# Optimization experiments

Measured on AMD Instinct MI355X. Metric: run time of the kernel, lower is better.

Reference implementation:

```python
import jax, jax.numpy as jnp
import numpy as np

SEQ_LEN = 8192
EMBED_DIM = 768
OUTPUT_DIM = 64


def setup_inputs() -> dict:
    key = jax.random.key(0)
    k_in, k_q, k_k, k_v = jax.random.split(key, 4)
    inputs = jax.random.normal(k_in, (SEQ_LEN, EMBED_DIM), dtype=jnp.float32)
    W_Q = jax.random.normal(k_q, (EMBED_DIM, OUTPUT_DIM), dtype=jnp.float32)
    W_K = jax.random.normal(k_k, (EMBED_DIM, OUTPUT_DIM), dtype=jnp.float32)
    W_V = jax.random.normal(k_v, (EMBED_DIM, OUTPUT_DIM), dtype=jnp.float32)
    return {"inputs": inputs, "W_Q": W_Q, "W_K": W_K, "W_V": W_V}


def reference(inputs, W_Q, W_K, W_V):
    # inputs: [N, E]; weights: [E, D]
    queries = inputs @ W_Q              # [N, D]
    keys = inputs @ W_K                 # [N, D]
    values = inputs @ W_V               # [N, D]
    scale = values.shape[-1] ** 0.5     # sqrt(output_dim), as in the original
    scores = queries @ keys.T           # [N, N] -- full score matrix, as original
    weights = jax.nn.softmax(scores / scale, axis=-1)
    context = weights @ values          # [N, D]
    return context
```

## Files before the change

### kernel.cpp

```cpp
#include <hip/hip_runtime.h>
#include <hip/hip_fp16.h>

#define N_SEQ 8192
#define E_DIM 768
#define D_OUT 64
#define PADK 68
#define SCALE_LOG2 0.18033688011112042f

typedef __attribute__((ext_vector_type(8)))  short s16x8;
typedef __attribute__((ext_vector_type(4)))  float f32x4;
typedef __attribute__((ext_vector_type(16))) float f32x16;

static __device__ __forceinline__ unsigned short f2bf(float f) {
    union { float f; unsigned int u; } v; v.f = f;
    unsigned int r = v.u + 0x7FFFu + ((v.u >> 16) & 1u);
    return (unsigned short)(r >> 16);
}
static __device__ __forceinline__ float bf2f(unsigned short h) {
    union { float f; unsigned int u; } v; v.u = ((unsigned int)h) << 16; return v.f;
}
static __device__ __forceinline__ unsigned int packbf(float a, float b) {
    union { float f; unsigned int u; } x, y; x.f = a; y.f = b;
    return (y.u & 0xFFFF0000u) | (x.u >> 16);
}
static __device__ __forceinline__ s16x8 gfrag(const unsigned short* p) {
    union { uint4 u; s16x8 s; } r; r.u = *(const uint4*)p; return r.s;
}
static __device__ __forceinline__ s16x8 ldsfrag(const unsigned short* p) {
    union { uint2 u[2]; s16x8 s; } r;
    r.u[0] = *(const uint2*)(p);
    r.u[1] = *(const uint2*)(p + 4);
    return r.s;
}
static __device__ __forceinline__ void st32(unsigned short* d, uint4 a, uint4 b) {
    uint2* p = (uint2*)d;
    p[0] = make_uint2(a.x, a.y); p[1] = make_uint2(a.z, a.w);
    p[2] = make_uint2(b.x, b.y); p[3] = make_uint2(b.z, b.w);
}

__global__ __launch_bounds__(256) void prep_w(const float* __restrict__ WQ,
                                              const float* __restrict__ WK,
                                              const float* __restrict__ WV,
                                              unsigned short* __restrict__ Wthi,
                                              unsigned short* __restrict__ Wtlo) {
    int idx = blockIdx.x * 256 + threadIdx.x;
    if (idx >= 192 * E_DIM) return;
    int n = idx / E_DIM;
    int k = idx - n * E_DIM;
    float v;
    if (n < 64)       v = WQ[k * 64 + n];
    else if (n < 128) v = WK[k * 64 + (n - 64)];
    else              v = WV[k * 64 + (n - 128)];
    unsigned short hb = f2bf(v);
    Wthi[idx] = hb;
    Wtlo[idx] = f2bf(v - bf2f(hb));
}

__global__ __launch_bounds__(256, 2) void proj_qkv(const float* __restrict__ X,
                                                   const unsigned short* __restrict__ Wthi,
                                                   const unsigned short* __restrict__ Wtlo,
                                                   unsigned short* __restrict__ Qhi,
                                                   unsigned short* __restrict__ Qlo,
                                                   unsigned short* __restrict__ Khi,
                                                   unsigned short* __restrict__ Klo,
                                                   unsigned short* __restrict__ Vt) {
    int tid  = threadIdx.x;
    int wv   = tid >> 6;
    int lane = tid & 63;
    int id   = blockIdx.x * 4 + wv;
    int mt   = id >> 2;
    int c    = id & 3;
    int m0 = mt * 16, n0 = c * 16;
    int lr = lane & 15, lk = lane >> 4;

    f32x4 aQ, aK, aV;
    #pragma unroll
    for (int i = 0; i < 4; ++i) { aQ[i] = 0.f; aK[i] = 0.f; aV[i] = 0.f; }

    const float*          xp  = X    + (size_t)(m0 + lr) * E_DIM + lk * 8;
    const unsigned short* wqh = Wthi + (size_t)(n0 + lr) * E_DIM + lk * 8;
    const unsigned short* wql = Wtlo + (size_t)(n0 + lr) * E_DIM + lk * 8;
    const unsigned short* wkh = Wthi + (size_t)(64 + n0 + lr) * E_DIM + lk * 8;
    const unsigned short* wkl = Wtlo + (size_t)(64 + n0 + lr) * E_DIM + lk * 8;
    const unsigned short* wvh = Wthi + (size_t)(128 + n0 + lr) * E_DIM + lk * 8;

    #pragma unroll 2
    for (int ks = 0; ks < E_DIM / 32; ++ks) {
        int kb = ks * 32;
        float4 x0 = *(const float4*)(xp + kb);
        float4 x1 = *(const float4*)(xp + kb + 4);
        s16x8 bqh = gfrag(wqh + kb);
        s16x8 bql = gfrag(wql + kb);
        s16x8 bkh = gfrag(wkh + kb);
        s16x8 bkl = gfrag(wkl + kb);
        s16x8 bvh = gfrag(wvh + kb);
        float xs[8] = { x0.x, x0.y, x0.z, x0.w, x1.x, x1.y, x1.z, x1.w };
        union { unsigned short u[8]; s16x8 s; } ah, al;
        #pragma unroll
        for (int i = 0; i < 8; ++i) {
            unsigned short hb = f2bf(xs[i]);
            ah.u[i] = hb;
            al.u[i] = f2bf(xs[i] - bf2f(hb));
        }
        aQ = __builtin_amdgcn_mfma_f32_16x16x32_bf16(ah.s, bqh, aQ, 0, 0, 0);
        aK = __builtin_amdgcn_mfma_f32_16x16x32_bf16(ah.s, bkh, aK, 0, 0, 0);
        aV = __builtin_amdgcn_mfma_f32_16x16x32_bf16(ah.s, bvh, aV, 0, 0, 0);
        aQ = __builtin_amdgcn_mfma_f32_16x16x32_bf16(ah.s, bql, aQ, 0, 0, 0);
        aK = __builtin_amdgcn_mfma_f32_16x16x32_bf16(ah.s, bkl, aK, 0, 0, 0);
        aQ = __builtin_amdgcn_mfma_f32_16x16x32_bf16(al.s, bqh, aQ, 0, 0, 0);
        aK = __builtin_amdgcn_mfma_f32_16x16x32_bf16(al.s, bkh, aK, 0, 0, 0);
    }

    #pragma unroll
    for (int r = 0; r < 4; ++r) {
        int grow = m0 + lk * 4 + r, gcol = n0 + lr;
        float q = aQ[r] * SCALE_LOG2;
        unsigned short hb = f2bf(q);
        Qhi[(size_t)grow * 64 + gcol] = hb;
        Qlo[(size_t)grow * 64 + gcol] = f2bf(q - bf2f(hb));
        float v = aK[r];
        hb = f2bf(v);
        Khi[(size_t)grow * 64 + gcol] = hb;
        Klo[(size_t)grow * 64 + gcol] = f2bf(v - bf2f(hb));
    }
    ushort4 pk;
    pk.x = f2bf(aV[0]); pk.y = f2bf(aV[1]);
    pk.z = f2bf(aV[2]); pk.w = f2bf(aV[3]);
    *(ushort4*)(Vt + (size_t)(n0 + lr) * N_SEQ + m0 + lk * 4) = pk;
}

__global__ __launch_bounds__(256, 3) void attn(const unsigned short* __restrict__ Qhi,
                                               const unsigned short* __restrict__ Qlo,
                                               const unsigned short* __restrict__ Khi,
                                               const unsigned short* __restrict__ Klo,
                                               const unsigned short* __restrict__ Vt,
                                               unsigned short* __restrict__ Opart,
                                               float* __restrict__ mpart,
                                               float* __restrict__ lpart,
                                               int chunk) {
    __shared__ unsigned short sK[128 * PADK];
    __shared__ unsigned short sV [64 * PADK];

    int tid = threadIdx.x, wv = tid >> 6, lane = tid & 63;
    int lrow = lane & 31, lh = lane >> 5;
    int c = blockIdx.x, qb = blockIdx.y;
    int q0 = qb * 128 + wv * 32;

    s16x8 qh[4], ql[4];
    #pragma unroll
    for (int ks = 0; ks < 4; ++ks) {
        int kb = ks * 16 + lh * 8;
        qh[ks] = gfrag(Qhi + (size_t)(q0 + lrow) * 64 + kb);
        ql[ks] = gfrag(Qlo + (size_t)(q0 + lrow) * 64 + kb);
    }

    f32x16 O0, O1;
    #pragma unroll
    for (int i = 0; i < 16; ++i) { O0[i] = 0.f; O1[i] = 0.f; }
    float mrow = -1e30f, lrun = 0.f;

    int steps = chunk >> 6;
    int srow = tid >> 2, sseg = tid & 3;

    uint4 rA0, rA1, rB0, rB1, rC0, rC1;
    {
        int j1 = c * chunk;
        const uint4* ps = (const uint4*)(Khi + ((size_t)(j1 + srow) * 64 + sseg * 16));
        rA0 = ps[0]; rA1 = ps[1];
        ps = (const uint4*)(Klo + ((size_t)(j1 + srow) * 64 + sseg * 16));
        rB0 = ps[0]; rB1 = ps[1];
        ps = (const uint4*)(Vt + ((size_t)srow * N_SEQ + j1 + sseg * 16));
        rC0 = ps[0]; rC1 = ps[1];
    }

    for (int it = 0; it < steps; ++it) {
        __syncthreads();
        st32(sK + srow * PADK + sseg * 16, rA0, rA1);
        st32(sK + (64 + srow) * PADK + sseg * 16, rB0, rB1);
        st32(sV + srow * PADK + sseg * 16, rC0, rC1);
        __syncthreads();

        if (it + 1 < steps) {
            int j1 = c * chunk + (it + 1) * 64;
            const uint4* ps = (const uint4*)(Khi + ((size_t)(j1 + srow) * 64 + sseg * 16));
            rA0 = ps[0]; rA1 = ps[1];
            ps = (const uint4*)(Klo + ((size_t)(j1 + srow) * 64 + sseg * 16));
            rB0 = ps[0]; rB1 = ps[1];
            ps = (const uint4*)(Vt + ((size_t)srow * N_SEQ + j1 + sseg * 16));
            rC0 = ps[0]; rC1 = ps[1];
        }

        f32x16 s0, s1;
        #pragma unroll
        for (int i = 0; i < 16; ++i) { s0[i] = 0.f; s1[i] = 0.f; }
        #pragma unroll
        for (int ks = 0; ks < 4; ++ks) {
            int kb = ks * 16 + lh * 8;
            s16x8 b0h = ldsfrag(sK + (size_t)lrow * PADK + kb);
            s16x8 b0l = ldsfrag(sK + (size_t)(64 + lrow) * PADK + kb);
            s0 = __builtin_amdgcn_mfma_f32_32x32x16_bf16(b0h, qh[ks], s0, 0, 0, 0);
            s0 = __builtin_amdgcn_mfma_f32_32x32x16_bf16(b0l, qh[ks], s0, 0, 0, 0);
            s0 = __builtin_amdgcn_mfma_f32_32x32x16_bf16(b0h, ql[ks], s0, 0, 0, 0);
            s16x8 b1h = ldsfrag(sK + (size_t)(32 + lrow) * PADK + kb);
            s16x8 b1l = ldsfrag(sK + (size_t)(96 + lrow) * PADK + kb);
            s1 = __builtin_amdgcn_mfma_f32_32x32x16_bf16(b1h, qh[ks], s1, 0, 0, 0);
            s1 = __builtin_amdgcn_mfma_f32_32x32x16_bf16(b1l, qh[ks], s1, 0, 0, 0);
            s1 = __builtin_amdgcn_mfma_f32_32x32x16_bf16(b1h, ql[ks], s1, 0, 0, 0);
        }

        float rm = s0[0];
        #pragma unroll
        for (int i = 1; i < 16; ++i) rm = fmaxf(rm, s0[i]);
        #pragma unroll
        for (int i = 0; i < 16; ++i) rm = fmaxf(rm, s1[i]);
        rm = fmaxf(rm, __shfl_xor(rm, 32, 64));
        float mn  = fmaxf(mrow, rm);
        float alf = exp2f(mrow - mn);
        mrow = mn;

        float psum = 0.f;
        #pragma unroll
        for (int i = 0; i < 16; ++i) { s0[i] = exp2f(s0[i] - mn); psum += s0[i]; }
        #pragma unroll
        for (int i = 0; i < 16; ++i) { s1[i] = exp2f(s1[i] - mn); psum += s1[i]; }
        lrun = lrun * alf + psum;

        unsigned int I[16], J[16];
        #pragma unroll
        for (int q4 = 0; q4 < 4; ++q4) {
            I[2 * q4]     = packbf(s0[4 * q4],     s0[4 * q4 + 1]);
            I[2 * q4 + 1] = packbf(s0[4 * q4 + 2], s0[4 * q4 + 3]);
            I[8 + 2 * q4]     = packbf(s1[4 * q4],     s1[4 * q4 + 1]);
            I[8 + 2 * q4 + 1] = packbf(s1[4 * q4 + 2], s1[4 * q4 + 3]);
        }
        #pragma unroll
        for (int i = 0; i < 16; ++i) J[i] = (unsigned int)__shfl_xor((int)I[i], 32, 64);
        s16x8 a[4];
        #pragma unroll
        for (int ks = 0; ks < 4; ++ks) {
            int b = (ks >> 1) * 8 + (ks & 1) * 4;
            union { unsigned int u[4]; s16x8 s; } fa;
            fa.u[0] = lh ? J[b + 2] : I[b];
            fa.u[1] = lh ? J[b + 3] : I[b + 1];
            fa.u[2] = lh ? I[b + 2] : J[b];
            fa.u[3] = lh ? I[b + 3] : J[b + 1];
            a[ks] = fa.s;
        }

        #pragma unroll
        for (int r = 0; r < 16; ++r) {
            int qr = (r & 3) + 8 * (r >> 2) + 4 * lh;
            float af = __shfl(alf, qr, 64);
            O0[r] *= af; O1[r] *= af;
        }

        #pragma unroll
        for (int ks = 0; ks < 4; ++ks) {
            int kb = ks * 16 + lh * 8;
            s16x8 b0 = ldsfrag(sV + (size_t)lrow * PADK + kb);
            s16x8 b1 = ldsfrag(sV + (size_t)(32 + lrow) * PADK + kb);
            O0 = __builtin_amdgcn_mfma_f32_32x32x16_bf16(a[ks], b0, O0, 0, 0, 0);
            O1 = __builtin_amdgcn_mfma_f32_32x32x16_bf16(a[ks], b1, O1, 0, 0, 0);
        }
    }

    #pragma unroll
    for (int r = 0; r < 16; ++r) {
        int row = (r & 3) + 8 * (r >> 2) + 4 * lh;
        int grow = q0 + row;
        size_t ob = ((size_t)c * N_SEQ + grow) * 64;
        Opart[ob + lrow]      = f2bf(O0[r]);
        Opart[ob + 32 + lrow] = f2bf(O1[r]);
    }
    float lfull = lrun + __shfl_xor(lrun, 32, 64);
    if (lane < 32) {
        int grow = q0 + lrow;
        mpart[c * N_SEQ + grow] = mrow;
        lpart[c * N_SEQ + grow] = lfull;
    }
}

__global__ __launch_bounds__(256) void combine(const unsigned short* __restrict__ Opart,
                                               const float* __restrict__ mpart,
                                               const float* __restrict__ lpart,
                                               float* __restrict__ out,
                                               int nsplit) {
    int idx = blockIdx.x * 256 + threadIdx.x;
    int row = idx >> 4, d4 = idx & 15;
    float M = -1e30f;
    for (int c = 0; c < nsplit; ++c) M = fmaxf(M, mpart[c * N_SEQ + row]);
    float4 num = make_float4(0.f, 0.f, 0.f, 0.f);
    float den = 0.f;
    for (int c = 0; c < nsplit; ++c) {
        float w = exp2f(mpart[c * N_SEQ + row] - M);
        den += w * lpart[c * N_SEQ + row];
        ushort4 o = ((const ushort4*)Opart)[((size_t)c * N_SEQ + row) * 16 + d4];
        num.x += w * bf2f(o.x); num.y += w * bf2f(o.y);
        num.z += w * bf2f(o.z); num.w += w * bf2f(o.w);
    }
    float inv = 1.0f / den;
    num.x *= inv; num.y *= inv; num.z *= inv; num.w *= inv;
    ((float4*)out)[idx] = num;
}

extern "C" void kernel_launch(void* const* d_in, const int* in_sizes, int n_in,
                              void* d_out, int out_size, void* d_ws, size_t ws_size,
                              hipStream_t stream) {
    const float* X  = (const float*)d_in[0];
    const float* WQ = (const float*)d_in[1];
    const float* WK = (const float*)d_in[2];
    const float* WV = (const float*)d_in[3];
    float* out = (float*)d_out;

    const size_t szQK = (size_t)N_SEQ * 64 * 2;
    const size_t szW  = (size_t)192 * E_DIM * 2;
    char* p = (char*)d_ws;
    unsigned short* Qhi = (unsigned short*)p; p += szQK;
    unsigned short* Qlo = (unsigned short*)p; p += szQK;
    unsigned short* Khi = (unsigned short*)p; p += szQK;
    unsigned short* Klo = (unsigned short*)p; p += szQK;
    unsigned short* Vt  = (unsigned short*)p; p += szQK;
    unsigned short* Wthi = (unsigned short*)p; p += szW;
    unsigned short* Wtlo = (unsigned short*)p; p += szW;
    size_t base = (size_t)(p - (char*)d_ws);
    size_t per  = (size_t)N_SEQ * 64 * 2 + 2 * (size_t)N_SEQ * 4;
    int nsplit = 16;
    while (nsplit > 1 && base + (size_t)nsplit * per > ws_size) nsplit >>= 1;
    float* mpart = (float*)p; p += (size_t)nsplit * N_SEQ * 4;
    float* lpart = (float*)p; p += (size_t)nsplit * N_SEQ * 4;
    unsigned short* Opart = (unsigned short*)p;

    int chunk = N_SEQ / nsplit;

    prep_w<<<(192 * E_DIM + 255) / 256, 256, 0, stream>>>(WQ, WK, WV, Wthi, Wtlo);
    proj_qkv<<<512, 256, 0, stream>>>(X, Wthi, Wtlo, Qhi, Qlo, Khi, Klo, Vt);
    attn<<<dim3(nsplit, N_SEQ / 128), 256, 0, stream>>>(Qhi, Qlo, Khi, Klo, Vt,
                                                        Opart, mpart, lpart, chunk);
    combine<<<(N_SEQ * 16 + 255) / 256, 256, 0, stream>>>(Opart, mpart, lpart, out, nsplit);
}
```

Measured before the change: 168.6 us.

## Stage X tile in LDS once per block and pre-swizzle weights into fragment order

The projection kernel now gives each block one 16-row tile of X. The tile is loaded cooperatively, split once into bf16 hi/lo and stored in shared memory in MFMA fragment order, so it is no longer converted redundantly in each of the four column waves. The weight prep kernel writes hi/lo weights in fragment-packed order, so each lane reads contiguous 16-byte chunks with coalesced access. This adds a block-wide barrier and 48KB of LDS per block, which may limit occupancy. The projection is a small part of the total time next to attention.

```diff
diff --git a/kernel.cpp b/kernel.cpp
--- a/kernel.cpp
+++ b/kernel.cpp
@@ -26,6 +26,9 @@
 static __device__ __forceinline__ s16x8 gfrag(const unsigned short* p) {
     union { uint4 u; s16x8 s; } r; r.u = *(const uint4*)p; return r.s;
 }
+static __device__ __forceinline__ s16x8 ldsq(const unsigned short* p) {
+    union { uint4 u; s16x8 s; } r; r.u = *(const uint4*)p; return r.s;
+}
 static __device__ __forceinline__ s16x8 ldsfrag(const unsigned short* p) {
     union { uint2 u[2]; s16x8 s; } r;
     r.u[0] = *(const uint2*)(p);
@@ -41,8 +44,8 @@
 __global__ __launch_bounds__(256) void prep_w(const float* __restrict__ WQ,
                                               const float* __restrict__ WK,
                                               const float* __restrict__ WV,
-                                              unsigned short* __restrict__ Wthi,
-                                              unsigned short* __restrict__ Wtlo) {
+                                              unsigned short* __restrict__ Wfh,
+                                              unsigned short* __restrict__ Wfl) {
     int idx = blockIdx.x * 256 + threadIdx.x;
     if (idx >= 192 * E_DIM) return;
     int n = idx / E_DIM;
@@ -51,64 +54,82 @@
     if (n < 64)       v = WQ[k * 64 + n];
     else if (n < 128) v = WK[k * 64 + (n - 64)];
     else              v = WV[k * 64 + (n - 128)];
+    int nblk = n >> 4, lr = n & 15;
+    int ks = k >> 5, lk = (k >> 3) & 3, e = k & 7;
+    size_t pos = ((size_t)(nblk * 24 + ks) * 64 + lk * 16 + lr) * 8 + e;
     unsigned short hb = f2bf(v);
-    Wthi[idx] = hb;
-    Wtlo[idx] = f2bf(v - bf2f(hb));
+    Wfh[pos] = hb;
+    Wfl[pos] = f2bf(v - bf2f(hb));
 }
 
 __global__ __launch_bounds__(256, 2) void proj_qkv(const float* __restrict__ X,
-                                                   const unsigned short* __restrict__ Wthi,
-                                                   const unsigned short* __restrict__ Wtlo,
+                                                   const unsigned short* __restrict__ Wfh,
+                                                   const unsigned short* __restrict__ Wfl,
                                                    unsigned short* __restrict__ Qhi,
                                                    unsigned short* __restrict__ Qlo,
                                                    unsigned short* __restrict__ Khi,
                                                    unsigned short* __restrict__ Klo,
                                                    unsigned short* __restrict__ Vt) {
+    __shared__ unsigned short sXh[24 * 64 * 8];
+    __shared__ unsigned short sXl[24 * 64 * 8];
+
     int tid  = threadIdx.x;
     int wv   = tid >> 6;
     int lane = tid & 63;
-    int id   = blockIdx.x * 4 + wv;
-    int mt   = id >> 2;
-    int c    = id & 3;
-    int m0 = mt * 16, n0 = c * 16;
+    int mt   = blockIdx.x;
+    int m0 = mt * 16, n0 = wv * 16;
     int lr = lane & 15, lk = lane >> 4;
 
+    {
+        const float4* xb = (const float4*)(X + (size_t)m0 * E_DIM);
+        #pragma unroll
+        for (int it = 0; it < 12; ++it) {
+            int f4 = it * 256 + tid;
+            int r  = f4 / 192;
+            int kb4 = (f4 - r * 192) * 4;
+            float4 v = xb[f4];
+            int ksx = kb4 >> 5, lkx = (kb4 >> 3) & 3, e0 = kb4 & 7;
+            int ln  = lkx * 16 + r;
+            ushort4 hi, lo;
+            hi.x = f2bf(v.x); lo.x = f2bf(v.x - bf2f(hi.x));
+            hi.y = f2bf(v.y); lo.y = f2bf(v.y - bf2f(hi.y));
+            hi.z = f2bf(v.z); lo.z = f2bf(v.z - bf2f(hi.z));
+            hi.w = f2bf(v.w); lo.w = f2bf(v.w - bf2f(hi.w));
+            int p = (ksx * 64 + ln) * 8 + e0;
+            *(ushort4*)(sXh + p) = hi;
+            *(ushort4*)(sXl + p) = lo;
+        }
+    }
+    __syncthreads();
+
     f32x4 aQ, aK, aV;
     #pragma unroll
     for (int i = 0; i < 4; ++i) { aQ[i] = 0.f; aK[i] = 0.f; aV[i] = 0.f; }
 
-    const float*          xp  = X    + (size_t)(m0 + lr) * E_DIM + lk * 8;
-    const unsigned short* wqh = Wthi + (size_t)(n0 + lr) * E_DIM + lk * 8;
-    const unsigned short* wql = Wtlo + (size_t)(n0 + lr) * E_DIM + lk * 8;
-    const unsigned short* wkh = Wthi + (size_t)(64 + n0 + lr) * E_DIM + lk * 8;
-    const unsigned short* wkl = Wtlo + (size_t)(64 + n0 + lr) * E_DIM + lk * 8;
-    const unsigned short* wvh = Wthi + (size_t)(128 + n0 + lr) * E_DIM + lk * 8;
+    const unsigned short* wq = Wfh + ((size_t)(wv * 24) * 64 + lane) * 8;
+    const unsigned short* wqL = Wfl + ((size_t)(wv * 24) * 64 + lane) * 8;
+    const unsigned short* wk = Wfh + ((size_t)((4 + wv) * 24) * 64 + lane) * 8;
+    const unsigned short* wkL = Wfl + ((size_t)((4 + wv) * 24) * 64 + lane) * 8;
+    const unsigned short* wvp = Wfh + ((size_t)((8 + wv) * 24) * 64 + lane) * 8;
 
     #pragma unroll 2
-    for (int ks = 0; ks < E_DIM / 32; ++ks) {
-        int kb = ks * 32;
-        float4 x0 = *(const float4*)(xp + kb);
-        float4 x1 = *(const float4*)(xp + kb + 4);
-        s16x8 bqh = gfrag(wqh + kb);
-        s16x8 bql = gfrag(wql + kb);
-        s16x8 bkh = gfrag(wkh + kb);
-        s16x8 bkl = gfrag(wkl + kb);
-        s16x8 bvh = gfrag(wvh + kb);
-        float xs[8] = { x0.x, x0.y, x0.z, x0.w, x1.x, x1.y, x1.z, x1.w };
-        union { unsigned short u[8]; s16x8 s; } ah, al;
-        #pragma unroll
-        for (int i = 0; i < 8; ++i) {
-            unsigned short hb = f2bf(xs[i]);
-            ah.u[i] = hb;
-            al.u[i] = f2bf(xs[i] - bf2f(hb));
-        }
-        aQ = __builtin_amdgcn_mfma_f32_16x16x32_bf16(ah.s, bqh, aQ, 0, 0, 0);
-        aK = __builtin_amdgcn_mfma_f32_16x16x32_bf16(ah.s, bkh, aK, 0, 0, 0);
-        aV = __builtin_amdgcn_mfma_f32_16x16x32_bf16(ah.s, bvh, aV, 0, 0, 0);
-        aQ = __builtin_amdgcn_mfma_f32_16x16x32_bf16(ah.s, bql, aQ, 0, 0, 0);
-        aK = __builtin_amdgcn_mfma_f32_16x16x32_bf16(ah.s, bkl, aK, 0, 0, 0);
-        aQ = __builtin_amdgcn_mfma_f32_16x16x32_bf16(al.s, bqh, aQ, 0, 0, 0);
-        aK = __builtin_amdgcn_mfma_f32_16x16x32_bf16(al.s, bkh, aK, 0, 0, 0);
+    for (int ks = 0; ks < 24; ++ks) {
+        const unsigned short* xs = sXh + (ks * 64 + lane) * 8;
+        s16x8 ah = ldsq(xs);
+        s16x8 al = ldsq(sXl + (ks * 64 + lane) * 8);
+        size_t wo = (size_t)ks * 64 * 8;
+        s16x8 bqh = gfrag(wq + wo);
+        s16x8 bql = gfrag(wqL + wo);
+        s16x8 bkh = gfrag(wk + wo);
+        s16x8 bkl = gfrag(wkL + wo);
+        s16x8 bvh = gfrag(wvp + wo);
+        aQ = __builtin_amdgcn_mfma_f32_16x16x32_bf16(ah, bqh, aQ, 0, 0, 0);
+        aK = __builtin_amdgcn_mfma_f32_16x16x32_bf16(ah, bkh, aK, 0, 0, 0);
+        aV = __builtin_amdgcn_mfma_f32_16x16x32_bf16(ah, bvh, aV, 0, 0, 0);
+        aQ = __builtin_amdgcn_mfma_f32_16x16x32_bf16(ah, bql, aQ, 0, 0, 0);
+        aK = __builtin_amdgcn_mfma_f32_16x16x32_bf16(ah, bkl, aK, 0, 0, 0);
+        aQ = __builtin_amdgcn_mfma_f32_16x16x32_bf16(al, bqh, aQ, 0, 0, 0);
+        aK = __builtin_amdgcn_mfma_f32_16x16x32_bf16(al, bkh, aK, 0, 0, 0);
     }
 
     #pragma unroll
@@ -320,8 +341,8 @@
     unsigned short* Khi = (unsigned short*)p; p += szQK;
     unsigned short* Klo = (unsigned short*)p; p += szQK;
     unsigned short* Vt  = (unsigned short*)p; p += szQK;
-    unsigned short* Wthi = (unsigned short*)p; p += szW;
-    unsigned short* Wtlo = (unsigned short*)p; p += szW;
+    unsigned short* Wfh = (unsigned short*)p; p += szW;
+    unsigned short* Wfl = (unsigned short*)p; p += szW;
     size_t base = (size_t)(p - (char*)d_ws);
     size_t per  = (size_t)N_SEQ * 64 * 2 + 2 * (size_t)N_SEQ * 4;
     int nsplit = 16;
@@ -332,8 +353,8 @@
 
     int chunk = N_SEQ / nsplit;
 
-    prep_w<<<(192 * E_DIM + 255) / 256, 256, 0, stream>>>(WQ, WK, WV, Wthi, Wtlo);
-    proj_qkv<<<512, 256, 0, stream>>>(X, Wthi, Wtlo, Qhi, Qlo, Khi, Klo, Vt);
+    prep_w<<<(192 * E_DIM + 255) / 256, 256, 0, stream>>>(WQ, WK, WV, Wfh, Wfl);
+    proj_qkv<<<512, 256, 0, stream>>>(X, Wfh, Wfl, Qhi, Qlo, Khi, Klo, Vt);
     attn<<<dim3(nsplit, N_SEQ / 128), 256, 0, stream>>>(Qhi, Qlo, Khi, Klo, Vt,
                                                         Opart, mpart, lpart, chunk);
     combine<<<(N_SEQ * 16 + 255) / 256, 256, 0, stream>>>(Opart, mpart, lpart, out, nsplit);
```

Result: faster. 144.1 us, median of 3 (-14.6%).
